# Kernel tuning notes

Measured on AMD Instinct MI355X. Metric: run time of the kernel, lower is better.

Reference implementation:

```python
import jax, jax.numpy as jnp
import numpy as np


def setup_inputs() -> dict:
    key = jax.random.key(0)
    k1, = jax.random.split(key, 1)
    x = jax.random.normal(k1, (16, 512, 64, 64), dtype=jnp.float32)
    gamma = jnp.zeros((1,), dtype=jnp.float32)
    return {"x": x, "gamma": gamma}


def reference(x, gamma):
    B, C, H, W = x.shape
    q = x.reshape(B, C, H * W)              # B x C x N
    # energy: B x C x C  (channel-channel gram matrix)
    energy = jnp.einsum('bcn,bdn->bcd', q, q)
    # max-subtract transform: max over last dim minus energy
    energy_new = jnp.max(energy, axis=-1, keepdims=True) - energy
    attention = jax.nn.softmax(energy_new, axis=-1)  # B x C x C
    out = jnp.einsum('bcd,bdn->bcn', attention, q).reshape(B, C, H, W)
    return gamma * out + x
```

## Files before the change

### kernel.cpp

```cpp
#include <hip/hip_runtime.h>
#include <stdint.h>

#define B_ 16
#define C_ 512
#define N_ 4096

typedef float f32x4 __attribute__((ext_vector_type(4)));
typedef __bf16 bf16x8 __attribute__((ext_vector_type(8)));

static __device__ __forceinline__ unsigned short f2bf(float f) {
    unsigned int u = __float_as_uint(f);
    u += 0x7fffu + ((u >> 16) & 1u);
    return (unsigned short)(u >> 16);
}

static __device__ __forceinline__ void gload_lds16(const void* g, void* l) {
    __builtin_amdgcn_global_load_lds(
        (__attribute__((address_space(1))) unsigned int*)(g),
        (__attribute__((address_space(3))) unsigned int*)(l),
        16, 0, 0);
}

__global__ __launch_bounds__(256)
void convert_transpose(const float* __restrict__ x,
                       unsigned short* __restrict__ q16,
                       unsigned short* __restrict__ qt16) {
    __shared__ unsigned short tile[64][72];
    int b  = blockIdx.z;
    int c0 = blockIdx.y * 64, n0 = blockIdx.x * 64;
    int tx = threadIdx.x & 15, ty = threadIdx.x >> 4;

    const float*    xb  = x    + ((size_t)b * C_ + c0) * N_ + n0;
    unsigned short* qb  = q16  + ((size_t)b * C_ + c0) * N_ + n0;
    unsigned short* qtb = qt16 + ((size_t)b * N_ + n0) * C_ + c0;

#pragma unroll
    for (int s = 0; s < 4; ++s) {
        int rr = s * 16 + ty;
        float4 v = *(const float4*)(xb + (size_t)rr * N_ + tx * 4);
        unsigned short h0 = f2bf(v.x), h1 = f2bf(v.y), h2 = f2bf(v.z), h3 = f2bf(v.w);
        tile[rr][tx * 4 + 0] = h0;
        tile[rr][tx * 4 + 1] = h1;
        tile[rr][tx * 4 + 2] = h2;
        tile[rr][tx * 4 + 3] = h3;
        ushort4 p; p.x = h0; p.y = h1; p.z = h2; p.w = h3;
        *(ushort4*)(qb + (size_t)rr * N_ + tx * 4) = p;
    }
    __syncthreads();
#pragma unroll
    for (int s = 0; s < 4; ++s) {
        int nr = s * 16 + ty;
        ushort4 p;
        p.x = tile[tx * 4 + 0][nr];
        p.y = tile[tx * 4 + 1][nr];
        p.z = tile[tx * 4 + 2][nr];
        p.w = tile[tx * 4 + 3][nr];
        *(ushort4*)(qtb + (size_t)nr * C_ + tx * 4) = p;
    }
}

template<int K>
__global__ __launch_bounds__(256)
void gemm_bt_energy(const unsigned short* __restrict__ q16,
                    float* __restrict__ energy) {
    int b = blockIdx.z;
    const unsigned short* Ab = q16 + (size_t)b * C_ * K;
    const unsigned short* Bb = Ab;
    int m0 = blockIdx.y * 128, n0 = blockIdx.x * 128;

    __shared__ unsigned short As[128 * 32];
    __shared__ unsigned short Bs[128 * 32];

    int t = threadIdx.x;
    int lane = t & 63, wave = t >> 6;
    int wm = (wave >> 1) * 64, wn = (wave & 1) * 64;
    int qd = lane >> 4, r = lane & 15;

    f32x4 acc[4][4] = {};

    for (int k0 = 0; k0 < K; k0 += 32) {
        __syncthreads();
#pragma unroll
        for (int i = 0; i < 2; ++i) {
            int o = (i * 256 + t) * 16;
            int mrow = o >> 6, inrow = o & 63;
            gload_lds16((const char*)Ab + (size_t)(m0 + mrow) * (K * 2) + k0 * 2 + inrow,
                        (char*)As + o);
            gload_lds16((const char*)Bb + (size_t)(n0 + mrow) * (K * 2) + k0 * 2 + inrow,
                        (char*)Bs + o);
        }
        __syncthreads();

        bf16x8 af[4], bfr[4];
#pragma unroll
        for (int i = 0; i < 4; ++i)
            af[i] = *(const bf16x8*)&As[(wm + i * 16 + r) * 32 + qd * 8];
#pragma unroll
        for (int j = 0; j < 4; ++j)
            bfr[j] = *(const bf16x8*)&Bs[(wn + j * 16 + r) * 32 + qd * 8];
#pragma unroll
        for (int i = 0; i < 4; ++i)
#pragma unroll
            for (int j = 0; j < 4; ++j)
                acc[i][j] = __builtin_amdgcn_mfma_f32_16x16x32_bf16(af[i], bfr[j], acc[i][j], 0, 0, 0);
    }

    float* Db = energy + (size_t)b * C_ * C_;
#pragma unroll
    for (int i = 0; i < 4; ++i)
#pragma unroll
        for (int j = 0; j < 4; ++j) {
            int row = m0 + wm + i * 16 + qd * 4;
            int col = n0 + wn + j * 16 + r;
#pragma unroll
            for (int rr = 0; rr < 4; ++rr)
                Db[(size_t)(row + rr) * C_ + col] = acc[i][j][rr];
        }
}

__global__ __launch_bounds__(256)
void softmax_neg(const float* __restrict__ energy, unsigned short* __restrict__ att) {
    size_t row = blockIdx.x;
    const float* e = energy + row * C_;
    int t = threadIdx.x;

    float e0 = e[t], e1 = e[t + 256];
    float m = fminf(e0, e1);
#pragma unroll
    for (int off = 32; off > 0; off >>= 1) m = fminf(m, __shfl_down(m, off, 64));
    __shared__ float red[8];
    if ((t & 63) == 0) red[t >> 6] = m;
    __syncthreads();
    m = fminf(fminf(red[0], red[1]), fminf(red[2], red[3]));

    float p0 = __expf(m - e0), p1 = __expf(m - e1);
    float s = p0 + p1;
#pragma unroll
    for (int off = 32; off > 0; off >>= 1) s += __shfl_down(s, off, 64);
    if ((t & 63) == 0) red[4 + (t >> 6)] = s;
    __syncthreads();
    s = red[4] + red[5] + red[6] + red[7];
    float inv = 1.0f / s;

    att[row * C_ + t]       = f2bf(p0 * inv);
    att[row * C_ + t + 256] = f2bf(p1 * inv);
}

__global__ __launch_bounds__(256)
void gemm_bt_out(const unsigned short* __restrict__ att,
                 const unsigned short* __restrict__ qt16,
                 const float* __restrict__ x,
                 const float* __restrict__ gamma,
                 float* __restrict__ y) {
    const int K = 512;
    int b = blockIdx.z;
    const unsigned short* Ab = att  + (size_t)b * C_ * K;
    const unsigned short* Bb = qt16 + (size_t)b * N_ * K;
    int m0 = blockIdx.y * 128;
    int n0 = blockIdx.x * 128;

    __shared__ unsigned short As[128 * 32];
    __shared__ unsigned short Bs[128 * 32];

    int t = threadIdx.x;
    int lane = t & 63, wave = t >> 6;
    int wm = (wave >> 1) * 64, wn = (wave & 1) * 64;
    int qd = lane >> 4, r = lane & 15;

    f32x4 acc[4][4] = {};

    for (int k0 = 0; k0 < K; k0 += 32) {
        __syncthreads();
#pragma unroll
        for (int i = 0; i < 2; ++i) {
            int o = (i * 256 + t) * 16;
            int mrow = o >> 6, inrow = o & 63;
            gload_lds16((const char*)Ab + (size_t)(m0 + mrow) * (K * 2) + k0 * 2 + inrow,
                        (char*)As + o);
            gload_lds16((const char*)Bb + (size_t)(n0 + mrow) * (K * 2) + k0 * 2 + inrow,
                        (char*)Bs + o);
        }
        __syncthreads();

        bf16x8 af[4], bfr[4];
#pragma unroll
        for (int i = 0; i < 4; ++i)
            af[i] = *(const bf16x8*)&As[(wm + i * 16 + r) * 32 + qd * 8];
#pragma unroll
        for (int j = 0; j < 4; ++j)
            bfr[j] = *(const bf16x8*)&Bs[(wn + j * 16 + r) * 32 + qd * 8];
#pragma unroll
        for (int i = 0; i < 4; ++i)
#pragma unroll
            for (int j = 0; j < 4; ++j)
                acc[i][j] = __builtin_amdgcn_mfma_f32_16x16x32_bf16(af[i], bfr[j], acc[i][j], 0, 0, 0);
    }

    float g = gamma[0];
    const float* xb = x + (size_t)b * C_ * N_;
    float*       yb = y + (size_t)b * C_ * N_;
#pragma unroll
    for (int i = 0; i < 4; ++i)
#pragma unroll
        for (int j = 0; j < 4; ++j) {
            int row = m0 + wm + i * 16 + qd * 4;
            int col = n0 + wn + j * 16 + r;
#pragma unroll
            for (int rr = 0; rr < 4; ++rr) {
                size_t idx = (size_t)(row + rr) * N_ + col;
                yb[idx] = g * acc[i][j][rr] + xb[idx];
            }
        }
}

extern "C" void kernel_launch(void* const* d_in, const int* in_sizes, int n_in,
                              void* d_out, int out_size, void* d_ws, size_t ws_size,
                              hipStream_t stream) {
    const float* x     = (const float*)d_in[0];
    const float* gamma = (const float*)d_in[1];
    float*       y     = (float*)d_out;

    char* ws = (char*)d_ws;
    unsigned short* q16   = (unsigned short*)(ws);
    unsigned short* qt16  = (unsigned short*)(ws + 67108864);
    unsigned short* att16 = (unsigned short*)(ws + 134217728);
    float*          energy= (float*)(ws + 142606336);

    convert_transpose<<<dim3(N_ / 64, C_ / 64, B_), dim3(256), 0, stream>>>(x, q16, qt16);
    gemm_bt_energy<N_><<<dim3(C_ / 128, C_ / 128, B_), dim3(256), 0, stream>>>(q16, energy);
    softmax_neg<<<dim3(B_ * C_), dim3(256), 0, stream>>>(energy, att16);
    gemm_bt_out<<<dim3(N_ / 128, C_ / 128, B_), dim3(256), 0, stream>>>(att16, qt16, x, gamma, y);
}
```

Before: 418.8 us.

## Split-K gram GEMM reading fp32 directly, drop q16 copy, transpose output GEMM

```diff
diff --git a/kernel.cpp b/kernel.cpp
--- a/kernel.cpp
+++ b/kernel.cpp
@@ -1,9 +1,11 @@
 #include <hip/hip_runtime.h>
+#include <hip/hip_bf16.h>
 #include <stdint.h>
 
 #define B_ 16
 #define C_ 512
 #define N_ 4096
+#define KS_ 4
 
 typedef float f32x4 __attribute__((ext_vector_type(4)));
 typedef __bf16 bf16x8 __attribute__((ext_vector_type(8)));
@@ -12,6 +14,15 @@
     unsigned int u = __float_as_uint(f);
     u += 0x7fffu + ((u >> 16) & 1u);
     return (unsigned short)(u >> 16);
+}
+
+static __device__ __forceinline__ uint2 f4_to_bf4(float4 v) {
+    __hip_bfloat162 lo = __float22bfloat162_rn(make_float2(v.x, v.y));
+    __hip_bfloat162 hi = __float22bfloat162_rn(make_float2(v.z, v.w));
+    uint2 r;
+    r.x = *reinterpret_cast<unsigned int*>(&lo);
+    r.y = *reinterpret_cast<unsigned int*>(&hi);
+    return r;
 }
 
 static __device__ __forceinline__ void gload_lds16(const void* g, void* l) {
@@ -23,28 +34,23 @@
 
 __global__ __launch_bounds__(256)
 void convert_transpose(const float* __restrict__ x,
-                       unsigned short* __restrict__ q16,
                        unsigned short* __restrict__ qt16) {
-    __shared__ unsigned short tile[64][72];
+    __shared__ unsigned short tile[64][65];
     int b  = blockIdx.z;
     int c0 = blockIdx.y * 64, n0 = blockIdx.x * 64;
     int tx = threadIdx.x & 15, ty = threadIdx.x >> 4;
 
     const float*    xb  = x    + ((size_t)b * C_ + c0) * N_ + n0;
-    unsigned short* qb  = q16  + ((size_t)b * C_ + c0) * N_ + n0;
     unsigned short* qtb = qt16 + ((size_t)b * N_ + n0) * C_ + c0;
 
 #pragma unroll
     for (int s = 0; s < 4; ++s) {
         int rr = s * 16 + ty;
         float4 v = *(const float4*)(xb + (size_t)rr * N_ + tx * 4);
-        unsigned short h0 = f2bf(v.x), h1 = f2bf(v.y), h2 = f2bf(v.z), h3 = f2bf(v.w);
-        tile[rr][tx * 4 + 0] = h0;
-        tile[rr][tx * 4 + 1] = h1;
-        tile[rr][tx * 4 + 2] = h2;
-        tile[rr][tx * 4 + 3] = h3;
-        ushort4 p; p.x = h0; p.y = h1; p.z = h2; p.w = h3;
-        *(ushort4*)(qb + (size_t)rr * N_ + tx * 4) = p;
+        tile[rr][tx * 4 + 0] = f2bf(v.x);
+        tile[rr][tx * 4 + 1] = f2bf(v.y);
+        tile[rr][tx * 4 + 2] = f2bf(v.z);
+        tile[rr][tx * 4 + 3] = f2bf(v.w);
     }
     __syncthreads();
 #pragma unroll
@@ -59,14 +65,108 @@
     }
 }
 
-template<int K>
-__global__ __launch_bounds__(256)
-void gemm_bt_energy(const unsigned short* __restrict__ q16,
-                    float* __restrict__ energy) {
+__global__ __launch_bounds__(256)
+void gemm_gram_splitk(const float* __restrict__ x, float* __restrict__ epart) {
+    int bz = blockIdx.z;
+    int b = bz >> 2, ks = bz & 3;
+    const int Kc = N_ / KS_;
+    const float* Xb = x + (size_t)b * C_ * N_ + (size_t)ks * Kc;
+    int m0 = blockIdx.y * 128, n0 = blockIdx.x * 128;
+
+    __shared__ unsigned short As[128 * 32];
+    __shared__ unsigned short Bs[128 * 32];
+
+    int t = threadIdx.x;
+    int lane = t & 63, wave = t >> 6;
+    int wm = (wave >> 1) * 64, wn = (wave & 1) * 64;
+    int qd = lane >> 4, r = lane & 15;
+
+    f32x4 acc[4][4] = {};
+
+    for (int k0 = 0; k0 < Kc; k0 += 32) {
+        __syncthreads();
+#pragma unroll
+        for (int p = 0; p < 4; ++p) {
+            int e = (p * 256 + t) * 4;
+            int row = e >> 5, col = e & 31;
+            float4 va = *(const float4*)(Xb + (size_t)(m0 + row) * N_ + k0 + col);
+            float4 vb = *(const float4*)(Xb + (size_t)(n0 + row) * N_ + k0 + col);
+            *(uint2*)&As[row * 32 + col] = f4_to_bf4(va);
+            *(uint2*)&Bs[row * 32 + col] = f4_to_bf4(vb);
+        }
+        __syncthreads();
+
+        bf16x8 af[4], bfr[4];
+#pragma unroll
+        for (int i = 0; i < 4; ++i)
+            af[i] = *(const bf16x8*)&As[(wm + i * 16 + r) * 32 + qd * 8];
+#pragma unroll
+        for (int j = 0; j < 4; ++j)
+            bfr[j] = *(const bf16x8*)&Bs[(wn + j * 16 + r) * 32 + qd * 8];
+#pragma unroll
+        for (int i = 0; i < 4; ++i)
+#pragma unroll
+            for (int j = 0; j < 4; ++j)
+                acc[i][j] = __builtin_amdgcn_mfma_f32_16x16x32_bf16(af[i], bfr[j], acc[i][j], 0, 0, 0);
+    }
+
+    float* Db = epart + (size_t)(ks * B_ + b) * C_ * C_;
+#pragma unroll
+    for (int i = 0; i < 4; ++i)
+#pragma unroll
+        for (int j = 0; j < 4; ++j) {
+            int cbase = m0 + wm + i * 16 + qd * 4;
+            int d     = n0 + wn + j * 16 + r;
+            *(f32x4*)(Db + (size_t)d * C_ + cbase) = acc[i][j];
+        }
+}
+
+__global__ __launch_bounds__(256)
+void softmax_neg4(const float* __restrict__ epart, unsigned short* __restrict__ att) {
+    size_t row = blockIdx.x;
+    const size_t slice = (size_t)B_ * C_ * C_;
+    const float* e = epart + row * C_;
+    int t = threadIdx.x;
+
+    float e0 = 0.f, e1 = 0.f;
+#pragma unroll
+    for (int s = 0; s < KS_; ++s) {
+        e0 += e[s * slice + t];
+        e1 += e[s * slice + t + 256];
+    }
+    float m = fminf(e0, e1);
+#pragma unroll
+    for (int off = 32; off > 0; off >>= 1) m = fminf(m, __shfl_down(m, off, 64));
+    __shared__ float red[8];
+    if ((t & 63) == 0) red[t >> 6] = m;
+    __syncthreads();
+    m = fminf(fminf(red[0], red[1]), fminf(red[2], red[3]));
+
+    float p0 = __expf(m - e0), p1 = __expf(m - e1);
+    float s = p0 + p1;
+#pragma unroll
+    for (int off = 32; off > 0; off >>= 1) s += __shfl_down(s, off, 64);
+    if ((t & 63) == 0) red[4 + (t >> 6)] = s;
+    __syncthreads();
+    s = red[4] + red[5] + red[6] + red[7];
+    float inv = 1.0f / s;
+
+    att[row * C_ + t]       = f2bf(p0 * inv);
+    att[row * C_ + t + 256] = f2bf(p1 * inv);
+}
+
+__global__ __launch_bounds__(256)
+void gemm_out_t(const unsigned short* __restrict__ att,
+                const unsigned short* __restrict__ qt16,
+                const float* __restrict__ x,
+                const float* __restrict__ gamma,
+                float* __restrict__ y) {
+    const int K = C_;
     int b = blockIdx.z;
-    const unsigned short* Ab = q16 + (size_t)b * C_ * K;
-    const unsigned short* Bb = Ab;
-    int m0 = blockIdx.y * 128, n0 = blockIdx.x * 128;
+    const unsigned short* Ab = qt16 + (size_t)b * N_ * C_;
+    const unsigned short* Bb = att  + (size_t)b * C_ * C_;
+    int m0 = blockIdx.x * 128;
+    int n0 = blockIdx.y * 128;
 
     __shared__ unsigned short As[128 * 32];
     __shared__ unsigned short Bs[128 * 32];
@@ -105,97 +205,6 @@
                 acc[i][j] = __builtin_amdgcn_mfma_f32_16x16x32_bf16(af[i], bfr[j], acc[i][j], 0, 0, 0);
     }
 
-    float* Db = energy + (size_t)b * C_ * C_;
-#pragma unroll
-    for (int i = 0; i < 4; ++i)
-#pragma unroll
-        for (int j = 0; j < 4; ++j) {
-            int row = m0 + wm + i * 16 + qd * 4;
-            int col = n0 + wn + j * 16 + r;
-#pragma unroll
-            for (int rr = 0; rr < 4; ++rr)
-                Db[(size_t)(row + rr) * C_ + col] = acc[i][j][rr];
-        }
-}
-
-__global__ __launch_bounds__(256)
-void softmax_neg(const float* __restrict__ energy, unsigned short* __restrict__ att) {
-    size_t row = blockIdx.x;
-    const float* e = energy + row * C_;
-    int t = threadIdx.x;
-
-    float e0 = e[t], e1 = e[t + 256];
-    float m = fminf(e0, e1);
-#pragma unroll
-    for (int off = 32; off > 0; off >>= 1) m = fminf(m, __shfl_down(m, off, 64));
-    __shared__ float red[8];
-    if ((t & 63) == 0) red[t >> 6] = m;
-    __syncthreads();
-    m = fminf(fminf(red[0], red[1]), fminf(red[2], red[3]));
-
-    float p0 = __expf(m - e0), p1 = __expf(m - e1);
-    float s = p0 + p1;
-#pragma unroll
-    for (int off = 32; off > 0; off >>= 1) s += __shfl_down(s, off, 64);
-    if ((t & 63) == 0) red[4 + (t >> 6)] = s;
-    __syncthreads();
-    s = red[4] + red[5] + red[6] + red[7];
-    float inv = 1.0f / s;
-
-    att[row * C_ + t]       = f2bf(p0 * inv);
-    att[row * C_ + t + 256] = f2bf(p1 * inv);
-}
-
-__global__ __launch_bounds__(256)
-void gemm_bt_out(const unsigned short* __restrict__ att,
-                 const unsigned short* __restrict__ qt16,
-                 const float* __restrict__ x,
-                 const float* __restrict__ gamma,
-                 float* __restrict__ y) {
-    const int K = 512;
-    int b = blockIdx.z;
-    const unsigned short* Ab = att  + (size_t)b * C_ * K;
-    const unsigned short* Bb = qt16 + (size_t)b * N_ * K;
-    int m0 = blockIdx.y * 128;
-    int n0 = blockIdx.x * 128;
-
-    __shared__ unsigned short As[128 * 32];
-    __shared__ unsigned short Bs[128 * 32];
-
-    int t = threadIdx.x;
-    int lane = t & 63, wave = t >> 6;
-    int wm = (wave >> 1) * 64, wn = (wave & 1) * 64;
-    int qd = lane >> 4, r = lane & 15;
-
-    f32x4 acc[4][4] = {};
-
-    for (int k0 = 0; k0 < K; k0 += 32) {
-        __syncthreads();
-#pragma unroll
-        for (int i = 0; i < 2; ++i) {
-            int o = (i * 256 + t) * 16;
-            int mrow = o >> 6, inrow = o & 63;
-            gload_lds16((const char*)Ab + (size_t)(m0 + mrow) * (K * 2) + k0 * 2 + inrow,
-                        (char*)As + o);
-            gload_lds16((const char*)Bb + (size_t)(n0 + mrow) * (K * 2) + k0 * 2 + inrow,
-                        (char*)Bs + o);
-        }
-        __syncthreads();
-
-        bf16x8 af[4], bfr[4];
-#pragma unroll
-        for (int i = 0; i < 4; ++i)
-            af[i] = *(const bf16x8*)&As[(wm + i * 16 + r) * 32 + qd * 8];
-#pragma unroll
-        for (int j = 0; j < 4; ++j)
-            bfr[j] = *(const bf16x8*)&Bs[(wn + j * 16 + r) * 32 + qd * 8];
-#pragma unroll
-        for (int i = 0; i < 4; ++i)
-#pragma unroll
-            for (int j = 0; j < 4; ++j)
-                acc[i][j] = __builtin_amdgcn_mfma_f32_16x16x32_bf16(af[i], bfr[j], acc[i][j], 0, 0, 0);
-    }
-
     float g = gamma[0];
     const float* xb = x + (size_t)b * C_ * N_;
     float*       yb = y + (size_t)b * C_ * N_;
@@ -203,13 +212,17 @@
     for (int i = 0; i < 4; ++i)
 #pragma unroll
         for (int j = 0; j < 4; ++j) {
-            int row = m0 + wm + i * 16 + qd * 4;
-            int col = n0 + wn + j * 16 + r;
-#pragma unroll
-            for (int rr = 0; rr < 4; ++rr) {
-                size_t idx = (size_t)(row + rr) * N_ + col;
-                yb[idx] = g * acc[i][j][rr] + xb[idx];
-            }
+            int nbase = m0 + wm + i * 16 + qd * 4;
+            int c     = n0 + wn + j * 16 + r;
+            size_t idx = (size_t)c * N_ + nbase;
+            float4 xv = *(const float4*)(xb + idx);
+            f32x4 a = acc[i][j];
+            float4 o;
+            o.x = g * a[0] + xv.x;
+            o.y = g * a[1] + xv.y;
+            o.z = g * a[2] + xv.z;
+            o.w = g * a[3] + xv.w;
+            *(float4*)(yb + idx) = o;
         }
 }
 
@@ -221,13 +234,12 @@
     float*       y     = (float*)d_out;
 
     char* ws = (char*)d_ws;
-    unsigned short* q16   = (unsigned short*)(ws);
-    unsigned short* qt16  = (unsigned short*)(ws + 67108864);
-    unsigned short* att16 = (unsigned short*)(ws + 134217728);
-    float*          energy= (float*)(ws + 142606336);
-
-    convert_transpose<<<dim3(N_ / 64, C_ / 64, B_), dim3(256), 0, stream>>>(x, q16, qt16);
-    gemm_bt_energy<N_><<<dim3(C_ / 128, C_ / 128, B_), dim3(256), 0, stream>>>(q16, energy);
-    softmax_neg<<<dim3(B_ * C_), dim3(256), 0, stream>>>(energy, att16);
-    gemm_bt_out<<<dim3(N_ / 128, C_ / 128, B_), dim3(256), 0, stream>>>(att16, qt16, x, gamma, y);
-}
+    unsigned short* qt16  = (unsigned short*)(ws);
+    unsigned short* att16 = (unsigned short*)(ws + 67108864);
+    float*          epart = (float*)(ws + 75497472);
+
+    convert_transpose<<<dim3(N_ / 64, C_ / 64, B_), dim3(256), 0, stream>>>(x, qt16);
+    gemm_gram_splitk<<<dim3(C_ / 128, C_ / 128, B_ * KS_), dim3(256), 0, stream>>>(x, epart);
+    softmax_neg4<<<dim3(B_ * C_), dim3(256), 0, stream>>>(epart, att16);
+    gemm_out_t<<<dim3(N_ / 128, C_ / 128, B_), dim3(256), 0, stream>>>(att16, qt16, x, gamma, y);
+}
```

Result: slower. 474.5 us (+13.3%).
